# Kernel tuning notes

Measured on AMD Instinct MI355X. Metric: run time of the kernel, lower is better.

Reference implementation:

```python
import jax, jax.numpy as jnp
import numpy as np

N = 8000       # n_sample (nodes)
F = 128        # n_feature
H = 128        # n_hidden
E = 256000     # edges (avg degree 32)
NPOOL = 3
K = 10         # propagation steps (args.k)
NC = 2         # n_class
ALPHA = 0.0    # Propagation(alpha=0.0)
CENTS = [400, 20, 1]   # node_pool = round(N**(1/NPOOL)) = 20; n_cent = round(prev/20)


def setup_inputs():
    key = jax.random.key(0)
    ks = jax.random.split(key, 40)
    def nrm(i, shape, scale=1.0):
        return jax.random.normal(ks[i], shape, jnp.float32) * scale
    x = nrm(0, (N, F))
    x_cov = nrm(1, (N, F))
    edge_rows = jax.random.randint(ks[2], (E,), 0, N, dtype=jnp.int32)
    edge_cols = jax.random.randint(ks[3], (E,), 0, N, dtype=jnp.int32)
    adj_vals = jax.random.uniform(ks[4], (E,), jnp.float32)
    raw = jax.random.uniform(ks[5], (E,), jnp.float32) + 0.1
    deg = jax.ops.segment_sum(raw, edge_rows, num_segments=N)
    norm_vals = raw / deg[edge_rows]   # row-normalized adjacency values
    inp = dict(x=x, x_cov=x_cov, edge_rows=edge_rows, edge_cols=edge_cols,
               adj_vals=adj_vals, norm_vals=norm_vals,
               bn_gamma=jnp.ones((F,), jnp.float32), bn_beta=jnp.zeros((F,), jnp.float32))
    i = 6
    for p, nc in enumerate(CENTS):
        inp['c%d_W1' % p] = nrm(i, (F, H), F ** -0.5); i += 1
        inp['c%d_b1' % p] = jnp.zeros((H,), jnp.float32)
        inp['c%d_W2' % p] = nrm(i, (H, nc), H ** -0.5); i += 1
        inp['c%d_b2' % p] = jnp.zeros((nc,), jnp.float32)
    inp['mW1'] = nrm(i, (F, H), F ** -0.5); i += 1
    inp['mb1'] = jnp.zeros((H,), jnp.float32)
    inp['a1'] = jnp.full((1,), 0.25, jnp.float32)   # PReLU slope
    inp['mW2'] = nrm(i, (H, H), H ** -0.5); i += 1
    inp['mb2'] = jnp.zeros((H,), jnp.float32)
    inp['a2'] = jnp.full((1,), 0.25, jnp.float32)
    inp['mW3'] = nrm(i, (H, NC), H ** -0.5); i += 1
    inp['mb3'] = jnp.zeros((NC,), jnp.float32)
    return inp


def _node_corr(z):
    # per-node decomposition of torch.corrcoef(z.T).sum(1):
    #   _node_corr(z).sum(0) == corrcoef(z.T).sum(1)
    zc = z - z.mean(0, keepdims=True)
    zc = zc / (jnp.linalg.norm(zc, axis=0, keepdims=True) + 1e-12)
    return zc * zc.sum(1, keepdims=True)   # [n, F]


def reference(x, x_cov, edge_rows, edge_cols, adj_vals, norm_vals, bn_gamma, bn_beta,
              c0_W1, c0_b1, c0_W2, c0_b2, c1_W1, c1_b1, c1_W2, c1_b2,
              c2_W1, c2_b1, c2_W2, c2_b2, mW1, mb1, a1, mW2, mb2, a2, mW3, mb3):
    # BatchNorm1d (training statistics, biased variance, eps=1e-5)
    mu, var = x.mean(0), x.var(0)
    x = (x - mu) / jnp.sqrt(var + 1e-5) * bn_gamma + bn_beta
    x0 = x

    # --- multi-level clustering / pooling (ClusteringLayer) ---
    cl_params = [(c0_W1, c0_b1, c0_W2, c0_b2), (c1_W1, c1_b1, c1_W2, c1_b2),
                 (c2_W1, c2_b1, c2_W2, c2_b2)]
    masks, corrs = [], []
    xc = x_cov
    for W1, b1, W2, b2 in cl_params:
        h = jax.nn.relu(xc @ W1 + b1)
        S = jax.nn.softmax(h @ W2 + b2, axis=-1)        # soft assignment [n_prev, n_cent]
        corrs.append(_node_corr(xc))                     # corr at the input level
        masks.append(S)
        xc = (S.T @ xc) / (S.sum(0)[:, None] + 1e-12)    # pooled centroid features
    corrs.append(_node_corr(x).sum(0))   # == torch.corrcoef(x.T).sum(1), shape [F]

    # --- gains: sigmoid(corr_{i+1} - normalize_adj(mask_i).T @ corr_i) ---
    gains = []
    for i in range(NPOOL):
        rn = masks[i] / (masks[i].sum(1, keepdims=True) + 1e-12)  # row-normalized (symmetric=False)
        gains.append(jax.nn.sigmoid(corrs[i + 1] - rn.T @ corrs[i]))

    # --- per-feature diagonal-masked sparse matmul chains, restricted to adj's edge set ---
    # projector to original nodes: P_i = masks[0] @ ... @ masks[i]
    P = [masks[0]]
    for i in range(1, NPOOL - 1):
        P.append(P[-1] @ masks[i])
    # (M M^T)[r,c] with M = P_i @ diag(g[:,j]) evaluated only on adj edges, all features at once
    def edge_mask(Pi, g):
        return jnp.einsum('ek,ek,kf->ef', Pi[edge_rows], Pi[edge_cols], g * g)  # [E, F]
    ms = [edge_mask(P[i], gains[i]) for i in reversed(range(NPOOL - 1))]  # i = NPOOL-2 .. 0
    ms = jnp.stack(ms, axis=0).transpose(2, 0, 1)   # [F, NPOOL-1, E]

    def per_feature(a, m_steps):   # sequential carry of adj over feature loop (matches torch)
        def inner(ai, mrow):
            ai = ai * mrow          # adj = adj * mask (elementwise on edge values)
            return ai, ai
        a, temps = jax.lax.scan(inner, a, m_steps)
        return a, temps.sum(0)      # adjs[j] = torch.sparse.sum(stack(temp), dim=0)
    _, adjs = jax.lax.scan(per_feature, adj_vals, ms)   # [F, E] edge values

    # --- diffusion propagation: x <- (1-alpha) * norm_adj @ x + alpha * x0, k times ---
    for _ in range(K):
        agg = jax.ops.segment_sum(norm_vals[:, None] * x[edge_cols], edge_rows, num_segments=N)
        x = (1.0 - ALPHA) * agg + ALPHA * x0

    # --- 3-layer MLP with PReLU + log_softmax ---
    prelu = lambda z, a: jnp.where(z >= 0, z, a * z)
    h = prelu(x @ mW1 + mb1, a1)
    h = prelu(h @ mW2 + mb2, a2)
    logits = h @ mW3 + mb3
    return jax.nn.log_softmax(logits, axis=1), adjs
```

## Files before the change

### kernel.cpp

```cpp
#include <hip/hip_runtime.h>
#include <hip/hip_bf16.h>

typedef __hip_bfloat16 bf16;
typedef __attribute__((ext_vector_type(8))) short s16x8;
typedef __attribute__((ext_vector_type(4))) float f32x4;

static constexpr int NN = 8000;
static constexpr int FF = 128;
static constexpr int EE = 256000;
static constexpr int NC0 = 400;
static constexpr int NC1 = 20;

__device__ __forceinline__ float b2f(bf16 v) { return __bfloat162float(v); }
__device__ __forceinline__ bf16 f2b(float v) { return __float2bfloat16(v); }
__device__ __forceinline__ short f2bs(float v) {
    bf16 h = __float2bfloat16(v);
    return __builtin_bit_cast(short, h);
}
__device__ __forceinline__ float ldw(float v) { return v; }
__device__ __forceinline__ float ldw(bf16 v) { return __bfloat162float(v); }

template <int NW>
__device__ __forceinline__ float block_sum(float v, float* sb) {
    #pragma unroll
    for (int o = 32; o > 0; o >>= 1) v += __shfl_down(v, o, 64);
    int t = threadIdx.x;
    if ((t & 63) == 0) sb[t >> 6] = v;
    __syncthreads();
    float s = 0.f;
    #pragma unroll
    for (int i = 0; i < NW; ++i) s += sb[i];
    __syncthreads();
    return s;
}

template <int NW>
__device__ __forceinline__ float block_max(float v, float* sb) {
    #pragma unroll
    for (int o = 32; o > 0; o >>= 1) v = fmaxf(v, __shfl_down(v, o, 64));
    int t = threadIdx.x;
    if ((t & 63) == 0) sb[t >> 6] = v;
    __syncthreads();
    float m = sb[0];
    #pragma unroll
    for (int i = 1; i < NW; ++i) m = fmaxf(m, sb[i]);
    __syncthreads();
    return m;
}

__global__ void k_fill_b16(bf16* __restrict__ p, float v, long n) {
    long i = (long)blockIdx.x * 256 + threadIdx.x;
    long stride = (long)gridDim.x * 256;
    for (; i < n; i += stride) p[i] = f2b(v);
}

__global__ void k_cvt_pad(const float* __restrict__ src, bf16* __restrict__ dst, int n) {
    int idx = blockIdx.x * 256 + threadIdx.x;
    if (idx < n) {
        int r = idx / 24, cc = idx - r * 24;
        dst[idx] = f2b(cc < 20 ? src[r * 20 + cc] : 0.f);
    }
}

__global__ void k_split(const float* __restrict__ src, bf16* __restrict__ dh,
                        bf16* __restrict__ dl, int n) {
    int i = blockIdx.x * 256 + threadIdx.x;
    if (i < n) {
        float v = src[i];
        bf16 h = f2b(v);
        dh[i] = h;
        dl[i] = f2b(v - b2f(h));
    }
}

__global__ __launch_bounds__(256)
void k_tsplit(const float* __restrict__ src, bf16* __restrict__ dh, bf16* __restrict__ dl,
              bf16* __restrict__ sh, bf16* __restrict__ sl, int M, int N) {
    __shared__ float t[32][33];
    int bx = blockIdx.x * 32, by = blockIdx.y * 32;
    int x = threadIdx.x;
    for (int y = threadIdx.y; y < 32; y += 8) {
        int m = by + y, n = bx + x;
        if (m < M && n < N) {
            float v = src[(long)m * N + n];
            t[y][x] = v;
            if (sh) {
                bf16 h = f2b(v);
                sh[(long)m * N + n] = h;
                sl[(long)m * N + n] = f2b(v - b2f(h));
            }
        }
    }
    __syncthreads();
    for (int y = threadIdx.y; y < 32; y += 8) {
        int n = bx + y, m = by + x;
        if (n < N && m < M) {
            float v = t[x][y];
            bf16 h = f2b(v);
            dh[(long)n * M + m] = h;
            dl[(long)n * M + m] = f2b(v - b2f(h));
        }
    }
}

__global__ __launch_bounds__(256)
void k_cstat(const float* __restrict__ x, const float* __restrict__ xcov,
             float* __restrict__ acc4) {
    __shared__ float sb[4][256];
    int t = threadIdx.x;
    int col = t & 127, half = t >> 7;
    int rend = min(NN, (blockIdx.x + 1) * 80);
    float sx = 0.f, qx = 0.f, sc = 0.f, qc = 0.f;
    for (int r = blockIdx.x * 80 + half; r < rend; r += 2) {
        float v = x[(long)r * FF + col];
        sx += v; qx += v * v;
        float w = xcov[(long)r * FF + col];
        sc += w; qc += w * w;
    }
    sb[0][t] = sx; sb[1][t] = qx; sb[2][t] = sc; sb[3][t] = qc;
    __syncthreads();
    if (t < 128) {
        atomicAdd(&acc4[0 * 128 + col], sb[0][t] + sb[0][t + 128]);
        atomicAdd(&acc4[1 * 128 + col], sb[1][t] + sb[1][t + 128]);
        atomicAdd(&acc4[2 * 128 + col], sb[2][t] + sb[2][t + 128]);
        atomicAdd(&acc4[3 * 128 + col], sb[3][t] + sb[3][t + 128]);
    }
}

__global__ void k_cfin(const float* __restrict__ acc4, const float* __restrict__ gamma,
                       const float* __restrict__ beta, float* __restrict__ bnsc,
                       float* __restrict__ bnsh, float* __restrict__ statmu,
                       float* __restrict__ statin) {
    int f = threadIdx.x;
    float s = acc4[f], q = acc4[128 + f];
    float mu = s / NN;
    float var = q / NN - mu * mu;
    if (var < 0.f) var = 0.f;
    float rstd = 1.f / sqrtf(var + 1e-5f);
    float sc = gamma[f] * rstd;
    bnsc[f] = sc;
    bnsh[f] = beta[f] - mu * sc;
    float s2 = acc4[256 + f], q2 = acc4[384 + f];
    float m2 = s2 / NN;
    float ss = q2 - s2 * m2;
    if (ss < 0.f) ss = 0.f;
    statmu[f] = m2;
    statin[f] = 1.f / (sqrtf(ss) + 1e-12f);
}

__global__ __launch_bounds__(128)
void k_nodecorr(const float* __restrict__ src, const float* __restrict__ mu,
                const float* __restrict__ invn, float* __restrict__ out) {
    __shared__ float sb[2];
    int n = blockIdx.x, t = threadIdx.x;
    float z = (src[n * FF + t] - mu[t]) * invn[t];
    float tot = block_sum<2>(z, sb);
    out[n * FF + t] = z * tot;
}

__global__ __launch_bounds__(256)
void k_softmax(float* __restrict__ p, int N) {
    __shared__ float sb[4];
    float* row = p + (long)blockIdx.x * N;
    int t = threadIdx.x;
    float m = -1e30f;
    for (int i = t; i < N; i += 256) m = fmaxf(m, row[i]);
    m = block_max<4>(m, sb);
    float s = 0.f;
    for (int i = t; i < N; i += 256) { float e = expf(row[i] - m); row[i] = e; s += e; }
    s = block_sum<4>(s, sb);
    float inv = 1.f / s;
    for (int i = t; i < N; i += 256) row[i] *= inv;
}

__global__ __launch_bounds__(256)
void k_softmax_b16(const float* __restrict__ src, bf16* __restrict__ dst, int N) {
    __shared__ float sb[4];
    const float* row = src + (long)blockIdx.x * N;
    bf16* orow = dst + (long)blockIdx.x * N;
    int t = threadIdx.x;
    float v0 = (t < N) ? row[t] : -1e30f;
    float v1 = (256 + t < N) ? row[256 + t] : -1e30f;
    float m = block_max<4>(fmaxf(v0, v1), sb);
    float e0 = (t < N) ? expf(v0 - m) : 0.f;
    float e1 = (256 + t < N) ? expf(v1 - m) : 0.f;
    float s = block_sum<4>(e0 + e1, sb);
    float inv = 1.f / s;
    if (t < N) orow[t] = f2b(e0 * inv);
    if (256 + t < N) orow[256 + t] = f2b(e1 * inv);
}

template <typename T>
__global__ __launch_bounds__(256)
void k_transpose(const T* __restrict__ src, T* __restrict__ dst, int M, int N) {
    __shared__ T t[32][33];
    int bx = blockIdx.x * 32, by = blockIdx.y * 32;
    int x = threadIdx.x;
    for (int y = threadIdx.y; y < 32; y += 8) {
        int m = by + y, n = bx + x;
        if (m < M && n < N) t[y][x] = src[(long)m * N + n];
    }
    __syncthreads();
    for (int y = threadIdx.y; y < 32; y += 8) {
        int n = bx + y, m = by + x;
        if (n < N && m < M) dst[(long)n * M + m] = t[x][y];
    }
}

template <typename T>
__global__ __launch_bounds__(256)
void k_colsum(const T* __restrict__ srcT, float* __restrict__ cs, int M) {
    __shared__ float sb[4];
    int r = blockIdx.x;
    float s = 0.f;
    for (int i = threadIdx.x; i < M; i += 256) s += ldw(srcT[(long)r * M + i]);
    s = block_sum<4>(s, sb);
    if (threadIdx.x == 0) cs[r] = s;
}

__global__ __launch_bounds__(256)
void k_gain0a(const float* __restrict__ T0, const float* __restrict__ cs0,
              float* __restrict__ xc1, float* __restrict__ mu, float* __restrict__ invn) {
    __shared__ float sb[4];
    int f = blockIdx.x;
    float s = 0.f, q = 0.f;
    for (int r = threadIdx.x; r < NC0; r += 256) {
        float v = T0[r * 128 + f] / (cs0[r] + 1e-12f);
        xc1[r * 128 + f] = v;
        s += v; q += v * v;
    }
    s = block_sum<4>(s, sb);
    q = block_sum<4>(q, sb);
    if (threadIdx.x == 0) {
        float m = s / NC0;
        float ss = q - s * m;
        if (ss < 0.f) ss = 0.f;
        mu[f] = m;
        invn[f] = 1.f / (sqrtf(ss) + 1e-12f);
    }
}

__global__ __launch_bounds__(128)
void k_gain0b(const float* __restrict__ xc1, const float* __restrict__ mu,
              const float* __restrict__ invn, const float* __restrict__ T1,
              float* __restrict__ corr1, bf16* __restrict__ g0swz) {
    __shared__ float sb[2];
    int k = blockIdx.x, f = threadIdx.x;
    int ch = k >> 5, rem = k & 31, lhi = rem >> 3, ii = rem & 7;
    int idx = (((ch * 8) + (f >> 4)) * 64 + (lhi * 16 + (f & 15))) * 8 + ii;
    if (k >= NC0) { g0swz[idx] = f2b(0.f); return; }
    float z = (xc1[k * 128 + f] - mu[f]) * invn[f];
    float tot = block_sum<2>(z, sb);
    float corr = z * tot;
    corr1[k * 128 + f] = corr;
    float d = corr - T1[k * 128 + f];
    float g = 1.f / (1.f + expf(-d));
    g0swz[idx] = f2b(g * g);
}

__global__ __launch_bounds__(256)
void k_gain1(const float* __restrict__ T2, const float* __restrict__ cs1,
             const float* __restrict__ T3, bf16* __restrict__ g1swz) {
    __shared__ float xs[20][128];
    __shared__ float mu[128], invn[128];
    __shared__ float sb[4];
    int t = threadIdx.x;
    for (int i = t; i < 20 * 128; i += 256) {
        int r = i >> 7;
        xs[r][i & 127] = T2[i] / (cs1[r] + 1e-12f);
    }
    __syncthreads();
    if (t < 128) {
        float s = 0.f, q = 0.f;
        for (int r = 0; r < 20; ++r) { float v = xs[r][t]; s += v; q += v * v; }
        float m = s / 20.f;
        float ss = q - s * m;
        if (ss < 0.f) ss = 0.f;
        mu[t] = m;
        invn[t] = 1.f / (sqrtf(ss) + 1e-12f);
    }
    __syncthreads();
    for (int r = 0; r < 20; ++r) {
        float z = 0.f;
        if (t < 128) z = (xs[r][t] - mu[t]) * invn[t];
        float tot = block_sum<4>(z, sb);
        if (t < 128) {
            float corr = z * tot;
            float d = corr - T3[r * 128 + t];
            float g = 1.f / (1.f + expf(-d));
            int lhi = (r >> 3) & 3, ii = r & 7;
            g1swz[(((t >> 4) * 64) + (lhi * 16 + (t & 15))) * 8 + ii] = f2b(g * g);
        }
    }
    for (int i = t; i < 12 * 128; i += 256) {
        int k = 20 + (i >> 7), f = i & 127;
        int lhi = (k >> 3) & 3, ii = k & 7;
        g1swz[(((f >> 4) * 64) + (lhi * 16 + (f & 15))) * 8 + ii] = f2b(0.f);
    }
}

template <typename AT, typename WT>
__global__ __launch_bounds__(256)
void k_gemm(const AT* __restrict__ A, const WT* __restrict__ W,
            const float* __restrict__ bias, const float* __restrict__ slope,
            float* __restrict__ C, int M, int K, int N, int act) {
    __shared__ float As[16][68];
    __shared__ float Ws[16][68];
    int tid = threadIdx.x;
    int tx = tid & 15, ty = tid >> 4;
    int m0 = blockIdx.x * 64, n0 = blockIdx.y * 64;
    int KS = gridDim.z;
    int kchunk = ((K + KS * 16 - 1) / (KS * 16)) * 16;
    int kbeg = blockIdx.z * kchunk;
    int kend = min(K, kbeg + kchunk);
    float acc[4][4] = {};
    for (int k0 = kbeg; k0 < kend; k0 += 16) {
        __syncthreads();
        for (int idx = tid; idx < 1024; idx += 256) {
            int r = idx >> 4, kk = idx & 15;
            int m = m0 + r, k = k0 + kk;
            As[kk][r] = (m < M && k < kend) ? ldw(A[(long)m * K + k]) : 0.f;
        }
        for (int idx = tid; idx < 1024; idx += 256) {
            int kk = idx >> 6, n = idx & 63;
            int k = k0 + kk, nn = n0 + n;
            float wv = 0.f;
            if (k < kend && nn < N) wv = ldw(W[(long)k * N + nn]);
            Ws[kk][n] = wv;
        }
        __syncthreads();
        #pragma unroll
        for (int kk = 0; kk < 16; ++kk) {
            float4 a4 = *(const float4*)&As[kk][ty * 4];
            float4 b4 = *(const float4*)&Ws[kk][tx * 4];
            float av[4] = {a4.x, a4.y, a4.z, a4.w};
            float bv[4] = {b4.x, b4.y, b4.z, b4.w};
            #pragma unroll
            for (int i = 0; i < 4; ++i)
                #pragma unroll
                for (int j = 0; j < 4; ++j) acc[i][j] += av[i] * bv[j];
        }
    }
    if (KS > 1) {
        #pragma unroll
        for (int i = 0; i < 4; ++i) {
            int m = m0 + ty * 4 + i;
            if (m >= M) continue;
            #pragma unroll
            for (int j = 0; j < 4; ++j) {
                int n = n0 + tx * 4 + j;
                if (n >= N) continue;
                atomicAdd(&C[(long)m * N + n], acc[i][j]);
            }
        }
    } else {
        float sl = slope ? slope[0] : 0.f;
        #pragma unroll
        for (int i = 0; i < 4; ++i) {
            int m = m0 + ty * 4 + i;
            if (m >= M) continue;
            #pragma unroll
            for (int j = 0; j < 4; ++j) {
                int n = n0 + tx * 4 + j;
                if (n >= N) continue;
                float v = acc[i][j] + (bias ? bias[n] : 0.f);
                if (act == 1) v = fmaxf(v, 0.f);
                else if (act == 2) v = (v >= 0.f) ? v : sl * v;
                C[(long)m * N + n] = v;
            }
        }
    }
}

template <int PARTS>
__global__ __launch_bounds__(256)
void k_gmm(const bf16* __restrict__ Ah, const bf16* __restrict__ Al,
           const bf16* __restrict__ BTh, const bf16* __restrict__ BTl,
           const float* __restrict__ bias, const float* __restrict__ slope,
           float* __restrict__ C, int M, int K, int N, int act) {
    __shared__ __align__(16) short At[2][64 * 40];
    __shared__ __align__(16) short Bt[2][64 * 40];
    int tid = threadIdx.x;
    int m0 = blockIdx.x * 64, n0 = blockIdx.y * 64;
    int KS = gridDim.z;
    int kchunk = ((K + KS * 32 - 1) / (KS * 32)) * 32;
    int kbeg = blockIdx.z * kchunk;
    int kend = min(K, kbeg + kchunk);
    int r = tid >> 2, s = tid & 3;
    int l = tid & 63, w = tid >> 6;
    int c = l & 15, g = l >> 4;
    bool arow_ok = (m0 + r < M);
    bool brow_ok = (n0 + r < N);
    const short* ahp = (const short*)Ah + (long)(m0 + r) * K;
    const short* alp = (PARTS >= 3) ? (const short*)Al + (long)(m0 + r) * K : nullptr;
    const short* bhp = (const short*)BTh + (long)(n0 + r) * K;
    const short* blp = (PARTS >= 2) ? (const short*)BTl + (long)(n0 + r) * K : nullptr;
    short* aw = &At[0][r * 40 + 8 * s];
    short* bw = &Bt[0][r * 40 + 8 * s];
    const int afo = (16 * w + c) * 40 + 8 * g;
    f32x4 acc[4] = {};
    for (int k0 = kbeg; k0 < kend; k0 += 32) {
        __syncthreads();
        {
            int kk = k0 + 8 * s;
            bool kok = kk < kend;
            s16x8 av = {}, bv = {};
            if (arow_ok && kok) av = *(const s16x8*)(ahp + kk);
            if (brow_ok && kok) bv = *(const s16x8*)(bhp + kk);
            *(s16x8*)aw = av;
            *(s16x8*)bw = bv;
            if (PARTS >= 2) {
                s16x8 b2 = {};
                if (brow_ok && kok) b2 = *(const s16x8*)(blp + kk);
                *(s16x8*)(bw + 64 * 40) = b2;
            }
            if (PARTS >= 3) {
                s16x8 a2 = {};
                if (arow_ok && kok) a2 = *(const s16x8*)(alp + kk);
                *(s16x8*)(aw + 64 * 40) = a2;
            }
        }
        __syncthreads();
        s16x8 ah_ = *(const s16x8*)&At[0][afo];
        s16x8 al_;
        if (PARTS >= 3) al_ = *(const s16x8*)&At[1][afo];
        #pragma unroll
        for (int nt = 0; nt < 4; ++nt) {
            int bfo = (16 * nt + c) * 40 + 8 * g;
            s16x8 bh_ = *(const s16x8*)&Bt[0][bfo];
            acc[nt] = __builtin_amdgcn_mfma_f32_16x16x32_bf16(ah_, bh_, acc[nt], 0, 0, 0);
            if (PARTS >= 2) {
                s16x8 bl_ = *(const s16x8*)&Bt[1][bfo];
                acc[nt] = __builtin_amdgcn_mfma_f32_16x16x32_bf16(ah_, bl_, acc[nt], 0, 0, 0);
            }
            if (PARTS >= 3)
                acc[nt] = __builtin_amdgcn_mfma_f32_16x16x32_bf16(al_, bh_, acc[nt], 0, 0, 0);
        }
    }
    if (KS > 1) {
        #pragma unroll
        for (int nt = 0; nt < 4; ++nt) {
            int n = n0 + 16 * nt + c;
            if (n >= N) continue;
            #pragma unroll
            for (int q = 0; q < 4; ++q) {
                int m = m0 + 16 * w + 4 * g + q;
                if (m < M) atomicAdd(&C[(long)m * N + n], acc[nt][q]);
            }
        }
    } else {
        float sl = slope ? slope[0] : 0.f;
        #pragma unroll
        for (int nt = 0; nt < 4; ++nt) {
            int n = n0 + 16 * nt + c;
            if (n >= N) continue;
            float bv = bias ? bias[n] : 0.f;
            #pragma unroll
            for (int q = 0; q < 4; ++q) {
                int m = m0 + 16 * w + 4 * g + q;
                if (m >= M) continue;
                float v = acc[nt][q] + bv;
                if (act == 1) v = fmaxf(v, 0.f);
                else if (act == 2) v = (v >= 0.f) ? v : sl * v;
                C[(long)m * N + n] = v;
            }
        }
    }
}

__global__ __launch_bounds__(256)
void k_edge(const int* __restrict__ er, const int* __restrict__ ec,
            const float* __restrict__ adj,
            const bf16* __restrict__ S0b, const bf16* __restrict__ P1hp,
            const bf16* __restrict__ g0swz, const bf16* __restrict__ g1swz,
            bf16* __restrict__ outp, int E) {
    __shared__ __align__(16) short Ot[128 * 72];
    const int tid = threadIdx.x;
    const int e0 = blockIdx.x * 64;
    const int l = tid & 63, w = tid >> 6;
    const int c = l & 15, g = l >> 4;
    const int eb = 16 * w + (l >> 2), seg = l & 3;
    const int rn = er[e0 + eb], cn = ec[e0 + eb];
    const short* S0s = (const short*)S0b;
    const short* rrow = S0s + (long)rn * 400 + 8 * seg;
    const short* crow = S0s + (long)cn * 400 + 8 * seg;
    const int pa = ((((l & 15) << 2) + g) << 2);
    const s16x8* g0p = (const s16x8*)g0swz;
    f32x4 acc0[8] = {};
    f32x4 acc1[8] = {};
    s16x8 ar = *(const s16x8*)(rrow);
    s16x8 ac = *(const s16x8*)(crow);
    #pragma unroll 1
    for (int ch = 0; ch < 13; ++ch) {
        s16x8 nar, nac;
        if (ch < 12) {
            nar = *(const s16x8*)(rrow + 32 * (ch + 1));
            nac = *(const s16x8*)(crow + 32 * (ch + 1));
        }
        s16x8 wv;
        #pragma unroll
        for (int i = 0; i < 8; ++i) {
            float av = __uint_as_float(((unsigned)(unsigned short)ar[i]) << 16);
            float bv = __uint_as_float(((unsigned)(unsigned short)ac[i]) << 16);
            wv[i] = f2bs(av * bv);
        }
        int4 wvi = __builtin_bit_cast(int4, wv);
        int4 wfi;
        wfi.x = __builtin_amdgcn_ds_bpermute(pa, wvi.x);
        wfi.y = __builtin_amdgcn_ds_bpermute(pa, wvi.y);
        wfi.z = __builtin_amdgcn_ds_bpermute(pa, wvi.z);
        wfi.w = __builtin_amdgcn_ds_bpermute(pa, wvi.w);
        s16x8 wfrag = __builtin_bit_cast(s16x8, wfi);
        const s16x8* gc = g0p + (long)ch * 512 + l;
        #pragma unroll
        for (int t = 0; t < 8; ++t)
            acc0[t] = __builtin_amdgcn_mfma_f32_16x16x32_bf16(gc[t * 64], wfrag, acc0[t], 0, 0, 0);
        ar = nar; ac = nac;
    }
    {
        s16x8 wv = {};
        if (seg < 3) {
            const short* P1s = (const short*)P1hp;
            s16x8 pr = *(const s16x8*)(P1s + (long)rn * 24 + 8 * seg);
            s16x8 pc = *(const s16x8*)(P1s + (long)cn * 24 + 8 * seg);
            #pragma unroll
            for (int i = 0; i < 8; ++i) {
                float av = __uint_as_float(((unsigned)(unsigned short)pr[i]) << 16);
                float bv = __uint_as_float(((unsigned)(unsigned short)pc[i]) << 16);
                wv[i] = f2bs(av * bv);
            }
        }
        int4 wvi = __builtin_bit_cast(int4, wv);
        int4 wfi;
        wfi.x = __builtin_amdgcn_ds_bpermute(pa, wvi.x);
        wfi.y = __builtin_amdgcn_ds_bpermute(pa, wvi.y);
        wfi.z = __builtin_amdgcn_ds_bpermute(pa, wvi.z);
        wfi.w = __builtin_amdgcn_ds_bpermute(pa, wvi.w);
        s16x8 wfrag = __builtin_bit_cast(s16x8, wfi);
        const s16x8* g1p = (const s16x8*)g1swz;
        #pragma unroll
        for (int t = 0; t < 8; ++t)
            acc1[t] = __builtin_amdgcn_mfma_f32_16x16x32_bf16(g1p[t * 64 + l], wfrag, acc1[t], 0, 0, 0);
    }
    const int ecl = 16 * w + c;
    float pre = adj[e0 + ecl];
    #pragma unroll
    for (int t = 0; t < 8; ++t) {
        float m10 = acc0[t][0], m11 = acc0[t][1], m12 = acc0[t][2], m13 = acc0[t][3];
        float m00 = acc1[t][0], m01 = acc1[t][1], m02 = acc1[t][2], m03 = acc1[t][3];
        float q0 = m00 * m10, q1 = m01 * m11, q2 = m02 * m12, q3 = m03 * m13;
        float eq1 = q0, eq2 = q0 * q1, eq3 = eq2 * q2;
        float incg = eq3 * q3;
        float u = __shfl_up(incg, 16, 64); if (g >= 1) incg *= u;
        u = __shfl_up(incg, 32, 64); if (g >= 2) incg *= u;
        float exg = __shfl_up(incg, 16, 64); if (g == 0) exg = 1.f;
        float tot = __shfl(incg, 48 + c, 64);
        float base = pre * exg;
        pre *= tot;
        int fb = 16 * t + 4 * g;
        Ot[(fb + 0) * 72 + ecl] = f2bs(base * m00 * (1.f + m10));
        Ot[(fb + 1) * 72 + ecl] = f2bs(base * eq1 * m01 * (1.f + m11));
        Ot[(fb + 2) * 72 + ecl] = f2bs(base * eq2 * m02 * (1.f + m12));
        Ot[(fb + 3) * 72 + ecl] = f2bs(base * eq3 * m03 * (1.f + m13));
    }
    __syncthreads();
    const int fo = tid & 127, hf = tid >> 7;
    if (fo < 127 || e0 < 240000) {
        const short* lsrc = &Ot[fo * 72 + hf * 32];
        short* gdst = (short*)outp + (long)fo * E + e0 + hf * 32;
        #pragma unroll
        for (int q = 0; q < 4; ++q)
            *(s16x8*)(gdst + 8 * q) = *(const s16x8*)(lsrc + 8 * q);
    }
}

__global__ void k_count(const int* __restrict__ er, int* __restrict__ counts, int E) {
    int e = blockIdx.x * 256 + threadIdx.x;
    if (e < E) atomicAdd(&counts[er[e]], 1);
}

__global__ __launch_bounds__(256)
void k_scan(const int* __restrict__ counts, int* __restrict__ rs,
            int* __restrict__ cur, int R) {
    __shared__ int buf[2][256];
    int t = threadIdx.x;
    const int PER = 32;
    int b = t * PER;
    int s = 0;
    for (int i = 0; i < PER; ++i) {
        int idx = b + i;
        if (idx < R) s += counts[idx];
    }
    buf[0][t] = s;
    __syncthreads();
    int src = 0;
    for (int off = 1; off < 256; off <<= 1) {
        int v = buf[src][t];
        if (t >= off) v += buf[src][t - off];
        buf[1 - src][t] = v;
        __syncthreads();
        src = 1 - src;
    }
    int base = (t > 0) ? buf[src][t - 1] : 0;
    for (int i = 0; i < PER; ++i) {
        int idx = b + i;
        if (idx < R) {
            int c = counts[idx];
            rs[idx] = base;
            cur[idx] = base;
            base += c;
        }
    }
    if (t == 255) rs[R] = buf[src][255];
}

__global__ void k_scatter(const int* __restrict__ er, const int* __restrict__ ec,
                          const float* __restrict__ nv, int* __restrict__ cur,
                          int2* __restrict__ cpack, int E) {
    int e = blockIdx.x * 256 + threadIdx.x;
    if (e < E) {
        int r = er[e];
        int p = atomicAdd(&cur[r], 1);
        cpack[p] = make_int2(ec[e], __float_as_int(nv[e]));
    }
}

__global__ __launch_bounds__(256)
void k_spmv4(const int* __restrict__ rs, const int2* __restrict__ cpack,
             const float* __restrict__ xin, float* __restrict__ xout,
             const float* __restrict__ sc4, const float* __restrict__ sh4, int R) {
    int lane = threadIdx.x & 31;
    int r = blockIdx.x * 8 + (threadIdx.x >> 5);
    if (r >= R) return;
    int jb = rs[r], je = rs[r + 1];
    float4 acc = {0.f, 0.f, 0.f, 0.f};
    if (sc4) {
        float4 sc = ((const float4*)sc4)[lane];
        float4 sh = ((const float4*)sh4)[lane];
        for (int j = jb; j < je; ++j) {
            int2 cv = cpack[j];
            float v = __int_as_float(cv.y);
            float4 xv = ((const float4*)(xin + (long)cv.x * FF))[lane];
            acc.x += v * (xv.x * sc.x + sh.x);
            acc.y += v * (xv.y * sc.y + sh.y);
            acc.z += v * (xv.z * sc.z + sh.z);
            acc.w += v * (xv.w * sc.w + sh.w);
        }
    } else {
        int j = jb;
        for (; j + 4 <= je; j += 4) {
            int2 cv0 = cpack[j], cv1 = cpack[j + 1], cv2 = cpack[j + 2], cv3 = cpack[j + 3];
            float4 x0 = ((const float4*)(xin + (long)cv0.x * FF))[lane];
            float4 x1 = ((const float4*)(xin + (long)cv1.x * FF))[lane];
            float4 x2 = ((const float4*)(xin + (long)cv2.x * FF))[lane];
            float4 x3 = ((const float4*)(xin + (long)cv3.x * FF))[lane];
            float v0 = __int_as_float(cv0.y), v1 = __int_as_float(cv1.y);
            float v2 = __int_as_float(cv2.y), v3 = __int_as_float(cv3.y);
            acc.x += v0 * x0.x; acc.y += v0 * x0.y; acc.z += v0 * x0.z; acc.w += v0 * x0.w;
            acc.x += v1 * x1.x; acc.y += v1 * x1.y; acc.z += v1 * x1.z; acc.w += v1 * x1.w;
            acc.x += v2 * x2.x; acc.y += v2 * x2.y; acc.z += v2 * x2.z; acc.w += v2 * x2.w;
            acc.x += v3 * x3.x; acc.y += v3 * x3.y; acc.z += v3 * x3.z; acc.w += v3 * x3.w;
        }
        for (; j < je; ++j) {
            int2 cv = cpack[j];
            float v = __int_as_float(cv.y);
            float4 xv = ((const float4*)(xin + (long)cv.x * FF))[lane];
            acc.x += v * xv.x; acc.y += v * xv.y; acc.z += v * xv.z; acc.w += v * xv.w;
        }
    }
    ((float4*)(xout + (long)r * FF))[lane] = acc;
}

__global__ __launch_bounds__(256)
void k_fc128(const float* __restrict__ xin, const float* __restrict__ W,
             const float* __restrict__ b, const float* __restrict__ a,
             float* __restrict__ hout, int nblk) {
    __shared__ float Ws[16384];
    __shared__ float xs[2][128];
    int t = threadIdx.x;
    for (int i = t; i < 16384; i += 256) Ws[i] = W[i];
    float slope = a[0];
    int half = t >> 7, tt = t & 127;
    float bb = b[tt];
    __syncthreads();
    for (int n = blockIdx.x * 2 + half; n < NN; n += nblk * 2) {
        xs[half][tt] = xin[(long)n * FF + tt];
        __syncthreads();
        float a0 = 0.f, a1 = 0.f, a2 = 0.f, a3 = 0.f;
        #pragma unroll 8
        for (int k = 0; k < 128; k += 4) {
            a0 += xs[half][k + 0] * Ws[(k + 0) * 128 + tt];
            a1 += xs[half][k + 1] * Ws[(k + 1) * 128 + tt];
            a2 += xs[half][k + 2] * Ws[(k + 2) * 128 + tt];
            a3 += xs[half][k + 3] * Ws[(k + 3) * 128 + tt];
        }
        float acc = bb + ((a0 + a1) + (a2 + a3));
        hout[(long)n * FF + tt] = (acc >= 0.f) ? acc : slope * acc;
        __syncthreads();
    }
}

__global__ __launch_bounds__(256)
void k_mlp_tail(const float* __restrict__ hin, const float* __restrict__ W2,
                const float* __restrict__ b2, const float* __restrict__ a2,
                const float* __restrict__ W3, const float* __restrict__ b3,
                bf16* __restrict__ outA, bf16* __restrict__ outB, int nblk) {
    __shared__ float Ws[16384];
    __shared__ float xs[2][128];
    __shared__ float red[8];
    int t = threadIdx.x;
    for (int i = t; i < 16384; i += 256) Ws[i] = W2[i];
    float slope = a2[0];
    int half = t >> 7, tt = t & 127;
    float bb = b2[tt];
    float w30 = W3[tt * 2 + 0], w31 = W3[tt * 2 + 1];
    float b30 = b3[0], b31 = b3[1];
    __syncthreads();
    for (int n = blockIdx.x * 2 + half; n < NN; n += nblk * 2) {
        xs[half][tt] = hin[(long)n * FF + tt];
        __syncthreads();
        float a0 = 0.f, a1 = 0.f, a2_ = 0.f, a3 = 0.f;
        #pragma unroll 8
        for (int k = 0; k < 128; k += 4) {
            a0 += xs[half][k + 0] * Ws[(k + 0) * 128 + tt];
            a1 += xs[half][k + 1] * Ws[(k + 1) * 128 + tt];
            a2_ += xs[half][k + 2] * Ws[(k + 2) * 128 + tt];
            a3 += xs[half][k + 3] * Ws[(k + 3) * 128 + tt];
        }
        float acc = bb + ((a0 + a1) + (a2_ + a3));
        float h2 = (acc >= 0.f) ? acc : slope * acc;
        float l0 = h2 * w30, l1 = h2 * w31;
        #pragma unroll
        for (int o = 32; o > 0; o >>= 1) {
            l0 += __shfl_down(l0, o, 64);
            l1 += __shfl_down(l1, o, 64);
        }
        int wid = t >> 6;
        if ((t & 63) == 0) { red[wid] = l0; red[4 + wid] = l1; }
        __syncthreads();
        if (tt == 0) {
            float L0 = red[half * 2] + red[half * 2 + 1] + b30;
            float L1 = red[4 + half * 2] + red[4 + half * 2 + 1] + b31;
            float m = fmaxf(L0, L1);
            float lse = m + logf(expf(L0 - m) + expf(L1 - m));
            bf16 v0 = f2b(L0 - lse), v1 = f2b(L1 - lse);
            outA[n * 2 + 0] = v0; outA[n * 2 + 1] = v1;
            outB[n * 2 + 0] = v0; outB[n * 2 + 1] = v1;
        }
        __syncthreads();
    }
}

extern "C" void kernel_launch(void* const* d_in, const int* in_sizes, int n_in,
                              void* d_out, int out_size, void* d_ws, size_t ws_size,
                              hipStream_t stream) {
    const float* x     = (const float*)d_in[0];
    const float* xcov  = (const float*)d_in[1];
    const int*   erow  = (const int*)d_in[2];
    const int*   ecol  = (const int*)d_in[3];
    const float* adjv  = (const float*)d_in[4];
    const float* normv = (const float*)d_in[5];
    const float* gamma = (const float*)d_in[6];
    const float* beta  = (const float*)d_in[7];
    const float* c0W1 = (const float*)d_in[8];  const float* c0b1 = (const float*)d_in[9];
    const float* c0W2 = (const float*)d_in[10]; const float* c0b2 = (const float*)d_in[11];
    const float* c1W1 = (const float*)d_in[12]; const float* c1b1 = (const float*)d_in[13];
    const float* c1W2 = (const float*)d_in[14]; const float* c1b2 = (const float*)d_in[15];
    const float* mW1 = (const float*)d_in[20]; const float* mb1 = (const float*)d_in[21];
    const float* a1  = (const float*)d_in[22];
    const float* mW2 = (const float*)d_in[23]; const float* mb2 = (const float*)d_in[24];
    const float* a2  = (const float*)d_in[25];
    const float* mW3 = (const float*)d_in[26]; const float* mb3 = (const float*)d_in[27];

    char* B = (char*)d_out;
    bf16* logitsA = (bf16*)B;
    bf16* logitsB = (bf16*)(B + 32000);
    bf16* adjsOut = (bf16*)(B + 64000);

    auto ovl = [](const void* a, size_t an, const void* b, size_t bn) {
        const char* A = (const char*)a; const char* Bp = (const char*)b;
        return (A < Bp + bn) && (Bp < A + an);
    };
    size_t outBytes = (size_t)out_size * 2;
    static const int expSize[28] = {1024000,1024000,256000,256000,256000,256000,128,128,
                                    16384,128,51200,400, 16384,128,2560,20, 16384,128,128,1,
                                    16384,128,1, 16384,128,1, 256,2};
    int code = 0;
    if (n_in != 28) code = 200;
    else for (int i = 0; i < 28 && !code; ++i) if (in_sizes[i] != expSize[i]) code = 200;
    if (!code && ovl(d_ws, ws_size, d_out, outBytes)) code = 300;
    if (!code) {
        for (int i = 0; i < 28; ++i) {
            size_t bytes = (size_t)in_sizes[i] * 4;
            if (ovl(d_ws, ws_size, d_in[i], bytes)) { code = 400; break; }
            if (ovl(d_out, outBytes, d_in[i], bytes)) { code = 500; break; }
        }
    }
    if (!code && ws_size < (size_t)6935040) code = 600;
    if (code) {
        k_fill_b16<<<64, 256, 0, stream>>>(logitsA, (float)code, 16000);
        k_fill_b16<<<64, 256, 0, stream>>>(logitsB, (float)code, 16000);
        k_fill_b16<<<2048, 256, 0, stream>>>(adjsOut, 0.0f, (outBytes - 64000) / 2);
        return;
    }

    char* ws = (char*)d_ws;
    bf16*  S0b   = (bf16*)(ws + 0);
    bf16*  P1hp  = (bf16*)(ws + 6400000);
    bf16*  g0swz = (bf16*)(ws + 6784000);
    bf16*  g1swz = (bf16*)(ws + 6890496);

    char* S = B + 64000;
    float* xbn   = (float*)(S + 0);
    float* ping  = (float*)(S + 4096000);
    float* h0    = (float*)(S + 8192000);
    float* hh2   = (float*)(S + 12288000);
    float* S0f   = (float*)(S + 16384000);
    bf16*  S0Tb  = (bf16*)(S + 29184000);
    float* P1f   = (float*)(S + 35584000);
    int*   rs    = (int*)(S + 36224000);
    int*   cur   = (int*)(S + 36256016);
    int2*  cpack = (int2*)(S + 36288016);
    float* T0    = (float*)(S + 38400512);
    float* T1    = (float*)(S + 38605312);
    float* xc1   = (float*)(S + 38810112);
    float* corr1 = (float*)(S + 39014912);
    float* h1    = (float*)(S + 39219712);
    float* S1    = (float*)(S + 39424512);
    float* S1T   = (float*)(S + 39456512);
    float* T2    = (float*)(S + 39488512);
    float* T3    = (float*)(S + 39498752);
    float* cs0   = (float*)(S + 39529472);
    float* cs1   = (float*)(S + 39531072);
    float* bnsc  = (float*)(S + 39532032);
    float* bnsh  = (float*)(S + 39532544);
    float* statmu= (float*)(S + 39533056);
    float* statin= (float*)(S + 39533568);
    float* acc4  = (float*)(S + 39534080);
    bf16* xcovh  = (bf16*)(S + 39749120);
    bf16* xcovl  = (bf16*)(S + 41797120);
    bf16* xcovTh = (bf16*)(S + 43845120);
    bf16* xcovTl = (bf16*)(S + 45893120);
    bf16* hh2Th  = (bf16*)(S + 47941120);
    bf16* hh2Tl  = (bf16*)(S + 49989120);
    bf16* h0h    = (bf16*)(S + 52037120);
    bf16* h0l    = (bf16*)(S + 54085120);
    bf16* W1Th   = (bf16*)(S + 56133120);
    bf16* W1Tl   = (bf16*)(S + 56165888);
    bf16* W2Th   = (bf16*)(S + 56198656);
    bf16* W2Tl   = (bf16*)(S + 56301056);
    bf16* S1Th   = (bf16*)(S + 56403456);
    bf16* S1Tl   = (bf16*)(S + 56419456);

    hipMemsetAsync(acc4, 0, 4 * 128 * 4, stream);
    k_cstat<<<100, 256, 0, stream>>>(x, xcov, acc4);
    k_cfin<<<1, 128, 0, stream>>>(acc4, gamma, beta, bnsc, bnsh, statmu, statin);
    k_nodecorr<<<NN, 128, 0, stream>>>(xcov, statmu, statin, hh2);
    k_tsplit<<<dim3(4, 250), dim3(32, 8), 0, stream>>>(xcov, xcovTh, xcovTl, xcovh, xcovl, NN, FF);
    k_tsplit<<<dim3(4, 250), dim3(32, 8), 0, stream>>>(hh2, hh2Th, hh2Tl, nullptr, nullptr, NN, FF);
    k_tsplit<<<dim3(4, 4), dim3(32, 8), 0, stream>>>(c0W1, W1Th, W1Tl, nullptr, nullptr, 128, 128);
    k_tsplit<<<dim3(13, 4), dim3(32, 8), 0, stream>>>(c0W2, W2Th, W2Tl, nullptr, nullptr, 128, NC0);
    k_gmm<3><<<dim3(125, 2, 1), 256, 0, stream>>>(xcovh, xcovl, W1Th, W1Tl, c0b1, nullptr, h0, NN, 128, 128, 1);
    k_split<<<4000, 256, 0, stream>>>(h0, h0h, h0l, NN * FF);
    k_gmm<3><<<dim3(125, 7, 1), 256, 0, stream>>>(h0h, h0l, W2Th, W2Tl, c0b2, nullptr, S0f, NN, 128, NC0, 0);
    k_softmax_b16<<<NN, 256, 0, stream>>>(S0f, S0b, NC0);
    k_transpose<bf16><<<dim3(13, 250), dim3(32, 8), 0, stream>>>(S0b, S0Tb, NN, NC0);
    k_colsum<bf16><<<NC0, 256, 0, stream>>>(S0Tb, cs0, NN);
    hipMemsetAsync(T0, 0, NC0 * 128 * 4, stream);
    hipMemsetAsync(T1, 0, NC0 * 128 * 4, stream);
    k_gmm<2><<<dim3(7, 2, 16), 256, 0, stream>>>(S0Tb, nullptr, xcovTh, xcovTl, nullptr, nullptr, T0, NC0, NN, 128, 0);
    k_gmm<2><<<dim3(7, 2, 16), 256, 0, stream>>>(S0Tb, nullptr, hh2Th, hh2Tl, nullptr, nullptr, T1, NC0, NN, 128, 0);
    k_gain0a<<<128, 256, 0, stream>>>(T0, cs0, xc1, statmu, statin);
    k_gain0b<<<416, 128, 0, stream>>>(xc1, statmu, statin, T1, corr1, g0swz);
    k_gemm<float, float><<<dim3(7, 2, 1), 256, 0, stream>>>(xc1, c1W1, c1b1, nullptr, h1, NC0, 128, 128, 1);
    k_gemm<float, float><<<dim3(7, 1, 1), 256, 0, stream>>>(h1, c1W2, c1b2, nullptr, S1, NC0, 128, NC1, 0);
    k_softmax<<<NC0, 256, 0, stream>>>(S1, NC1);
    k_transpose<float><<<dim3(1, 13), dim3(32, 8), 0, stream>>>(S1, S1T, NC0, NC1);
    k_colsum<float><<<NC1, 256, 0, stream>>>(S1T, cs1, NC0);
    k_tsplit<<<dim3(1, 13), dim3(32, 8), 0, stream>>>(S1, S1Th, S1Tl, nullptr, nullptr, NC0, NC1);
    hipMemsetAsync(T2, 0, NC1 * 128 * 4, stream);
    hipMemsetAsync(T3, 0, NC1 * 128 * 4, stream);
    k_gemm<float, float><<<dim3(1, 2, 4), 256, 0, stream>>>(S1T, xc1, nullptr, nullptr, T2, NC1, NC0, 128, 0);
    k_gemm<float, float><<<dim3(1, 2, 4), 256, 0, stream>>>(S1T, corr1, nullptr, nullptr, T3, NC1, NC0, 128, 0);
    k_gain1<<<1, 256, 0, stream>>>(T2, cs1, T3, g1swz);
    k_gmm<2><<<dim3(125, 1, 1), 256, 0, stream>>>(S0b, nullptr, S1Th, S1Tl, nullptr, nullptr, P1f, NN, NC0, NC1, 0);
    k_cvt_pad<<<750, 256, 0, stream>>>(P1f, P1hp, NN * 24);
    hipMemsetAsync(cur, 0, NN * 4, stream);
    k_count<<<1000, 256, 0, stream>>>(erow, cur, EE);
    k_scan<<<1, 256, 0, stream>>>(cur, rs, cur, NN);
    k_scatter<<<1000, 256, 0, stream>>>(erow, ecol, normv, cur, cpack, EE);
    k_spmv4<<<1000, 256, 0, stream>>>(rs, cpack, x, xbn, bnsc, bnsh, NN);
    float* xa = xbn;
    float* xb = ping;
    for (int it = 1; it < 10; ++it) {
        k_spmv4<<<1000, 256, 0, stream>>>(rs, cpack, xa, xb, nullptr, nullptr, NN);
        float* t = xa; xa = xb; xb = t;
    }
    k_fc128<<<250, 256, 0, stream>>>(ping, mW1, mb1, a1, h0, 250);
    k_mlp_tail<<<250, 256, 0, stream>>>(h0, mW2, mb2, a2, mW3, mb3, logitsA, logitsB, 250);
    k_edge<<<EE / 64, 256, 0, stream>>>(erow, ecol, adjv, S0b, P1hp, g0swz, g1swz, adjsOut, EE);
}
```

Baseline: 803.0 us.

## Fuse split/pad into GEMM epilogues, colsum into transpose, unroll edge and spmv loops

Several independent changes. The hi/lo bf16 split of h0 and the bf16 pad of P1 move into the k_gmm epilogue, and the column sums move into the transpose kernel through atomics, which drops three kernels and their intermediate fp32 round trips. k_edge loads two chunks ahead with a macro-unrolled body and hoists the P1 and adj loads earlier to hide latency. The first spmv pass is unrolled by four to overlap gathers. The costs are more register pressure and atomic accumulation order that is no longer deterministic.

```diff
diff --git a/kernel.cpp b/kernel.cpp
--- a/kernel.cpp
+++ b/kernel.cpp
@@ -52,25 +52,6 @@
     long i = (long)blockIdx.x * 256 + threadIdx.x;
     long stride = (long)gridDim.x * 256;
     for (; i < n; i += stride) p[i] = f2b(v);
-}
-
-__global__ void k_cvt_pad(const float* __restrict__ src, bf16* __restrict__ dst, int n) {
-    int idx = blockIdx.x * 256 + threadIdx.x;
-    if (idx < n) {
-        int r = idx / 24, cc = idx - r * 24;
-        dst[idx] = f2b(cc < 20 ? src[r * 20 + cc] : 0.f);
-    }
-}
-
-__global__ void k_split(const float* __restrict__ src, bf16* __restrict__ dh,
-                        bf16* __restrict__ dl, int n) {
-    int i = blockIdx.x * 256 + threadIdx.x;
-    if (i < n) {
-        float v = src[i];
-        bf16 h = f2b(v);
-        dh[i] = h;
-        dl[i] = f2b(v - b2f(h));
-    }
 }
 
 __global__ __launch_bounds__(256)
@@ -192,8 +173,10 @@
 
 template <typename T>
 __global__ __launch_bounds__(256)
-void k_transpose(const T* __restrict__ src, T* __restrict__ dst, int M, int N) {
+void k_transpose(const T* __restrict__ src, T* __restrict__ dst, float* __restrict__ cs,
+                 int M, int N) {
     __shared__ T t[32][33];
+    __shared__ float cbuf[8][33];
     int bx = blockIdx.x * 32, by = blockIdx.y * 32;
     int x = threadIdx.x;
     for (int y = threadIdx.y; y < 32; y += 8) {
@@ -205,17 +188,23 @@
         int n = bx + y, m = by + x;
         if (n < N && m < M) dst[(long)n * M + m] = t[x][y];
     }
-}
-
-template <typename T>
-__global__ __launch_bounds__(256)
-void k_colsum(const T* __restrict__ srcT, float* __restrict__ cs, int M) {
-    __shared__ float sb[4];
-    int r = blockIdx.x;
-    float s = 0.f;
-    for (int i = threadIdx.x; i < M; i += 256) s += ldw(srcT[(long)r * M + i]);
-    s = block_sum<4>(s, sb);
-    if (threadIdx.x == 0) cs[r] = s;
+    if (cs) {
+        int ty = threadIdx.y;
+        int n = bx + x;
+        float p = 0.f;
+        if (n < N) {
+            for (int y = ty; y < 32; y += 8)
+                if (by + y < M) p += ldw(t[y][x]);
+        }
+        cbuf[ty][x] = p;
+        __syncthreads();
+        if (ty == 0 && n < N) {
+            float s = 0.f;
+            #pragma unroll
+            for (int i = 0; i < 8; ++i) s += cbuf[i][x];
+            atomicAdd(&cs[n], s);
+        }
+    }
 }
 
 __global__ __launch_bounds__(256)
@@ -377,7 +366,8 @@
 void k_gmm(const bf16* __restrict__ Ah, const bf16* __restrict__ Al,
            const bf16* __restrict__ BTh, const bf16* __restrict__ BTl,
            const float* __restrict__ bias, const float* __restrict__ slope,
-           float* __restrict__ C, int M, int K, int N, int act) {
+           float* __restrict__ C, bf16* __restrict__ Csh, bf16* __restrict__ Csl,
+           int padN, int M, int K, int N, int act) {
     __shared__ __align__(16) short At[2][64 * 40];
     __shared__ __align__(16) short Bt[2][64 * 40];
     int tid = threadIdx.x;
@@ -448,6 +438,39 @@
                 if (m < M) atomicAdd(&C[(long)m * N + n], acc[nt][q]);
             }
         }
+    } else if (Csh && Csl) {
+        float sl = slope ? slope[0] : 0.f;
+        #pragma unroll
+        for (int nt = 0; nt < 4; ++nt) {
+            int n = n0 + 16 * nt + c;
+            if (n >= N) continue;
+            float bv = bias ? bias[n] : 0.f;
+            #pragma unroll
+            for (int q = 0; q < 4; ++q) {
+                int m = m0 + 16 * w + 4 * g + q;
+                if (m >= M) continue;
+                float v = acc[nt][q] + bv;
+                if (act == 1) v = fmaxf(v, 0.f);
+                else if (act == 2) v = (v >= 0.f) ? v : sl * v;
+                bf16 hi = f2b(v);
+                Csh[(long)m * N + n] = hi;
+                Csl[(long)m * N + n] = f2b(v - b2f(hi));
+            }
+        }
+    } else if (Csh) {
+        #pragma unroll
+        for (int nt = 0; nt < 4; ++nt) {
+            int n = n0 + 16 * nt + c;
+            if (n >= padN) continue;
+            float bv = (bias && n < N) ? bias[n] : 0.f;
+            #pragma unroll
+            for (int q = 0; q < 4; ++q) {
+                int m = m0 + 16 * w + 4 * g + q;
+                if (m >= M) continue;
+                float v = (n < N) ? acc[nt][q] + bv : 0.f;
+                Csh[(long)m * padN + n] = f2b(v);
+            }
+        }
     } else {
         float sl = slope ? slope[0] : 0.f;
         #pragma unroll
@@ -467,6 +490,28 @@
         }
     }
 }
+
+#define KE_CHUNK(AR, AC, CH)                                                        \
+    {                                                                               \
+        s16x8 wv;                                                                   \
+        _Pragma("unroll")                                                           \
+        for (int i = 0; i < 8; ++i) {                                               \
+            float av = __uint_as_float(((unsigned)(unsigned short)(AR)[i]) << 16);  \
+            float bv = __uint_as_float(((unsigned)(unsigned short)(AC)[i]) << 16);  \
+            wv[i] = f2bs(av * bv);                                                  \
+        }                                                                           \
+        int4 wvi = __builtin_bit_cast(int4, wv);                                    \
+        int4 wfi;                                                                   \
+        wfi.x = __builtin_amdgcn_ds_bpermute(pa, wvi.x);                            \
+        wfi.y = __builtin_amdgcn_ds_bpermute(pa, wvi.y);                            \
+        wfi.z = __builtin_amdgcn_ds_bpermute(pa, wvi.z);                            \
+        wfi.w = __builtin_amdgcn_ds_bpermute(pa, wvi.w);                            \
+        s16x8 wfrag = __builtin_bit_cast(s16x8, wfi);                               \
+        const s16x8* gc = g0p + (long)(CH) * 512 + l;                               \
+        _Pragma("unroll")                                                           \
+        for (int t = 0; t < 8; ++t)                                                 \
+            acc0[t] = __builtin_amdgcn_mfma_f32_16x16x32_bf16(gc[t * 64], wfrag, acc0[t], 0, 0, 0); \
+    }
 
 __global__ __launch_bounds__(256)
 void k_edge(const int* __restrict__ er, const int* __restrict__ ec,
@@ -486,43 +531,38 @@
     const short* crow = S0s + (long)cn * 400 + 8 * seg;
     const int pa = ((((l & 15) << 2) + g) << 2);
     const s16x8* g0p = (const s16x8*)g0swz;
+    const int ecl = 16 * w + c;
+    float pre = adj[e0 + ecl];
+    s16x8 pr = {}, pc = {};
+    if (seg < 3) {
+        const short* P1s = (const short*)P1hp;
+        pr = *(const s16x8*)(P1s + (long)rn * 24 + 8 * seg);
+        pc = *(const s16x8*)(P1s + (long)cn * 24 + 8 * seg);
+    }
     f32x4 acc0[8] = {};
     f32x4 acc1[8] = {};
-    s16x8 ar = *(const s16x8*)(rrow);
-    s16x8 ac = *(const s16x8*)(crow);
+    s16x8 arA = *(const s16x8*)(rrow);
+    s16x8 acA = *(const s16x8*)(crow);
+    s16x8 arB = *(const s16x8*)(rrow + 32);
+    s16x8 acB = *(const s16x8*)(crow + 32);
     #pragma unroll 1
-    for (int ch = 0; ch < 13; ++ch) {
-        s16x8 nar, nac;
-        if (ch < 12) {
-            nar = *(const s16x8*)(rrow + 32 * (ch + 1));
-            nac = *(const s16x8*)(crow + 32 * (ch + 1));
-        }
-        s16x8 wv;
-        #pragma unroll
-        for (int i = 0; i < 8; ++i) {
-            float av = __uint_as_float(((unsigned)(unsigned short)ar[i]) << 16);
-            float bv = __uint_as_float(((unsigned)(unsigned short)ac[i]) << 16);
-            wv[i] = f2bs(av * bv);
-        }
-        int4 wvi = __builtin_bit_cast(int4, wv);
-        int4 wfi;
-        wfi.x = __builtin_amdgcn_ds_bpermute(pa, wvi.x);
-        wfi.y = __builtin_amdgcn_ds_bpermute(pa, wvi.y);
-        wfi.z = __builtin_amdgcn_ds_bpermute(pa, wvi.z);
-        wfi.w = __builtin_amdgcn_ds_bpermute(pa, wvi.w);
-        s16x8 wfrag = __builtin_bit_cast(s16x8, wfi);
-        const s16x8* gc = g0p + (long)ch * 512 + l;
-        #pragma unroll
-        for (int t = 0; t < 8; ++t)
-            acc0[t] = __builtin_amdgcn_mfma_f32_16x16x32_bf16(gc[t * 64], wfrag, acc0[t], 0, 0, 0);
-        ar = nar; ac = nac;
-    }
+    for (int ch = 0; ch < 12; ch += 2) {
+        s16x8 nar = *(const s16x8*)(rrow + 32 * (ch + 2));
+        s16x8 nac = *(const s16x8*)(crow + 32 * (ch + 2));
+        KE_CHUNK(arA, acA, ch);
+        arA = nar; acA = nac;
+        s16x8 nbr = {}, nbc = {};
+        if (ch + 3 < 13) {
+            nbr = *(const s16x8*)(rrow + 32 * (ch + 3));
+            nbc = *(const s16x8*)(crow + 32 * (ch + 3));
+        }
+        KE_CHUNK(arB, acB, ch + 1);
+        arB = nbr; acB = nbc;
+    }
+    KE_CHUNK(arA, acA, 12);
     {
         s16x8 wv = {};
         if (seg < 3) {
-            const short* P1s = (const short*)P1hp;
-            s16x8 pr = *(const s16x8*)(P1s + (long)rn * 24 + 8 * seg);
-            s16x8 pc = *(const s16x8*)(P1s + (long)cn * 24 + 8 * seg);
             #pragma unroll
             for (int i = 0; i < 8; ++i) {
                 float av = __uint_as_float(((unsigned)(unsigned short)pr[i]) << 16);
@@ -542,8 +582,6 @@
         for (int t = 0; t < 8; ++t)
             acc1[t] = __builtin_amdgcn_mfma_f32_16x16x32_bf16(g1p[t * 64 + l], wfrag, acc1[t], 0, 0, 0);
     }
-    const int ecl = 16 * w + c;
-    float pre = adj[e0 + ecl];
     #pragma unroll
     for (int t = 0; t < 8; ++t) {
         float m10 = acc0[t][0], m11 = acc0[t][1], m12 = acc0[t][2], m13 = acc0[t][3];
@@ -573,6 +611,7 @@
             *(s16x8*)(gdst + 8 * q) = *(const s16x8*)(lsrc + 8 * q);
     }
 }
+#undef KE_CHUNK
 
 __global__ void k_count(const int* __restrict__ er, int* __restrict__ counts, int E) {
     int e = blockIdx.x * 256 + threadIdx.x;
@@ -637,7 +676,25 @@
     if (sc4) {
         float4 sc = ((const float4*)sc4)[lane];
         float4 sh = ((const float4*)sh4)[lane];
-        for (int j = jb; j < je; ++j) {
+        int j = jb;
+        for (; j + 4 <= je; j += 4) {
+            int2 cv0 = cpack[j], cv1 = cpack[j + 1], cv2 = cpack[j + 2], cv3 = cpack[j + 3];
+            float4 x0 = ((const float4*)(xin + (long)cv0.x * FF))[lane];
+            float4 x1 = ((const float4*)(xin + (long)cv1.x * FF))[lane];
+            float4 x2 = ((const float4*)(xin + (long)cv2.x * FF))[lane];
+            float4 x3 = ((const float4*)(xin + (long)cv3.x * FF))[lane];
+            float v0 = __int_as_float(cv0.y), v1 = __int_as_float(cv1.y);
+            float v2 = __int_as_float(cv2.y), v3 = __int_as_float(cv3.y);
+            acc.x += v0 * (x0.x * sc.x + sh.x) + v1 * (x1.x * sc.x + sh.x)
+                   + v2 * (x2.x * sc.x + sh.x) + v3 * (x3.x * sc.x + sh.x);
+            acc.y += v0 * (x0.y * sc.y + sh.y) + v1 * (x1.y * sc.y + sh.y)
+                   + v2 * (x2.y * sc.y + sh.y) + v3 * (x3.y * sc.y + sh.y);
+            acc.z += v0 * (x0.z * sc.z + sh.z) + v1 * (x1.z * sc.z + sh.z)
+                   + v2 * (x2.z * sc.z + sh.z) + v3 * (x3.z * sc.z + sh.z);
+            acc.w += v0 * (x0.w * sc.w + sh.w) + v1 * (x1.w * sc.w + sh.w)
+                   + v2 * (x2.w * sc.w + sh.w) + v3 * (x3.w * sc.w + sh.w);
+        }
+        for (; j < je; ++j) {
             int2 cv = cpack[j];
             float v = __int_as_float(cv.y);
             float4 xv = ((const float4*)(xin + (long)cv.x * FF))[lane];
@@ -817,7 +874,6 @@
     float* hh2   = (float*)(S + 12288000);
     float* S0f   = (float*)(S + 16384000);
     bf16*  S0Tb  = (bf16*)(S + 29184000);
-    float* P1f   = (float*)(S + 35584000);
     int*   rs    = (int*)(S + 36224000);
     int*   cur   = (int*)(S + 36256016);
     int2*  cpack = (int2*)(S + 36288016);
@@ -860,31 +916,34 @@
     k_tsplit<<<dim3(4, 250), dim3(32, 8), 0, stream>>>(hh2, hh2Th, hh2Tl, nullptr, nullptr, NN, FF);
     k_tsplit<<<dim3(4, 4), dim3(32, 8), 0, stream>>>(c0W1, W1Th, W1Tl, nullptr, nullptr, 128, 128);
     k_tsplit<<<dim3(13, 4), dim3(32, 8), 0, stream>>>(c0W2, W2Th, W2Tl, nullptr, nullptr, 128, NC0);
-    k_gmm<3><<<dim3(125, 2, 1), 256, 0, stream>>>(xcovh, xcovl, W1Th, W1Tl, c0b1, nullptr, h0, NN, 128, 128, 1);
-    k_split<<<4000, 256, 0, stream>>>(h0, h0h, h0l, NN * FF);
-    k_gmm<3><<<dim3(125, 7, 1), 256, 0, stream>>>(h0h, h0l, W2Th, W2Tl, c0b2, nullptr, S0f, NN, 128, NC0, 0);
+    k_gmm<3><<<dim3(125, 2, 1), 256, 0, stream>>>(xcovh, xcovl, W1Th, W1Tl, c0b1, nullptr,
+                                                  nullptr, h0h, h0l, 0, NN, 128, 128, 1);
+    k_gmm<3><<<dim3(125, 7, 1), 256, 0, stream>>>(h0h, h0l, W2Th, W2Tl, c0b2, nullptr,
+                                                  S0f, nullptr, nullptr, 0, NN, 128, NC0, 0);
     k_softmax_b16<<<NN, 256, 0, stream>>>(S0f, S0b, NC0);
-    k_transpose<bf16><<<dim3(13, 250), dim3(32, 8), 0, stream>>>(S0b, S0Tb, NN, NC0);
-    k_colsum<bf16><<<NC0, 256, 0, stream>>>(S0Tb, cs0, NN);
+    hipMemsetAsync(cs0, 0, NC0 * 4, stream);
+    k_transpose<bf16><<<dim3(13, 250), dim3(32, 8), 0, stream>>>(S0b, S0Tb, cs0, NN, NC0);
     hipMemsetAsync(T0, 0, NC0 * 128 * 4, stream);
     hipMemsetAsync(T1, 0, NC0 * 128 * 4, stream);
-    k_gmm<2><<<dim3(7, 2, 16), 256, 0, stream>>>(S0Tb, nullptr, xcovTh, xcovTl, nullptr, nullptr, T0, NC0, NN, 128, 0);
-    k_gmm<2><<<dim3(7, 2, 16), 256, 0, stream>>>(S0Tb, nullptr, hh2Th, hh2Tl, nullptr, nullptr, T1, NC0, NN, 128, 0);
+    k_gmm<2><<<dim3(7, 2, 16), 256, 0, stream>>>(S0Tb, nullptr, xcovTh, xcovTl, nullptr, nullptr,
+                                                 T0, nullptr, nullptr, 0, NC0, NN, 128, 0);
+    k_gmm<2><<<dim3(7, 2, 16), 256, 0, stream>>>(S0Tb, nullptr, hh2Th, hh2Tl, nullptr, nullptr,
+                                                 T1, nullptr, nullptr, 0, NC0, NN, 128, 0);
     k_gain0a<<<128, 256, 0, stream>>>(T0, cs0, xc1, statmu, statin);
     k_gain0b<<<416, 128, 0, stream>>>(xc1, statmu, statin, T1, corr1, g0swz);
     k_gemm<float, float><<<dim3(7, 2, 1), 256, 0, stream>>>(xc1, c1W1, c1b1, nullptr, h1, NC0, 128, 128, 1);
     k_gemm<float, float><<<dim3(7, 1, 1), 256, 0, stream>>>(h1, c1W2, c1b2, nullptr, S1, NC0, 128, NC1, 0);
     k_softmax<<<NC0, 256, 0, stream>>>(S1, NC1);
-    k_transpose<float><<<dim3(1, 13), dim3(32, 8), 0, stream>>>(S1, S1T, NC0, NC1);
-    k_colsum<float><<<NC1, 256, 0, stream>>>(S1T, cs1, NC0);
+    hipMemsetAsync(cs1, 0, NC1 * 4, stream);
+    k_transpose<float><<<dim3(1, 13), dim3(32, 8), 0, stream>>>(S1, S1T, cs1, NC0, NC1);
     k_tsplit<<<dim3(1, 13), dim3(32, 8), 0, stream>>>(S1, S1Th, S1Tl, nullptr, nullptr, NC0, NC1);
     hipMemsetAsync(T2, 0, NC1 * 128 * 4, stream);
     hipMemsetAsync(T3, 0, NC1 * 128 * 4, stream);
     k_gemm<float, float><<<dim3(1, 2, 4), 256, 0, stream>>>(S1T, xc1, nullptr, nullptr, T2, NC1, NC0, 128, 0);
     k_gemm<float, float><<<dim3(1, 2, 4), 256, 0, stream>>>(S1T, corr1, nullptr, nullptr, T3, NC1, NC0, 128, 0);
     k_gain1<<<1, 256, 0, stream>>>(T2, cs1, T3, g1swz);
-    k_gmm<2><<<dim3(125, 1, 1), 256, 0, stream>>>(S0b, nullptr, S1Th, S1Tl, nullptr, nullptr, P1f, NN, NC0, NC1, 0);
-    k_cvt_pad<<<750, 256, 0, stream>>>(P1f, P1hp, NN * 24);
+    k_gmm<2><<<dim3(125, 1, 1), 256, 0, stream>>>(S0b, nullptr, S1Th, S1Tl, nullptr, nullptr,
+                                                  nullptr, P1hp, nullptr, 24, NN, NC0, NC1, 0);
     hipMemsetAsync(cur, 0, NN * 4, stream);
     k_count<<<1000, 256, 0, stream>>>(erow, cur, EE);
     k_scan<<<1, 256, 0, stream>>>(cur, rs, cur, NN);
```

Measured after the change: 812.4 us. No clear change (+1.2%).
